# Optimization experiments

Hardware: AMD Instinct MI355X
Metric: run time of the kernel (lower is better)

Reference implementation:

```python
import jax, jax.numpy as jnp
import numpy as np

NEG_SLOPE = 0.2   # PyG GATConv default negative_slope
LN_EPS = 1e-5

B, N, D, HID, HEADS = 4, 10000, 128, 256, 2
F_HEAD = HID // HEADS  # 128
E_RAND = 160000


def setup_inputs() -> dict:
    key = jax.random.key(0)
    ks = jax.random.split(key, 12)
    src = jax.random.randint(ks[0], (E_RAND,), 0, N, dtype=jnp.int32)
    dst = jax.random.randint(ks[1], (E_RAND,), 0, N, dtype=jnp.int32)
    loops = jnp.arange(N, dtype=jnp.int32)  # PyG GATConv adds self-loops
    edge_index = jnp.stack([jnp.concatenate([src, loops]),
                            jnp.concatenate([dst, loops])])  # [2, 170000]
    feature = jax.random.normal(ks[2], (B, N, D), jnp.float32)

    def w(k, shape):
        return jax.random.normal(k, shape, jnp.float32) * 0.05

    return {
        "feature": feature,
        "edge_index": edge_index,
        # layer 1: in D=128 -> heads*F_HEAD = 256
        "W1": w(ks[3], (D, HEADS * F_HEAD)),
        "a_src1": w(ks[4], (HEADS, F_HEAD)),
        "a_dst1": w(ks[5], (HEADS, F_HEAD)),
        "b1": jnp.zeros((HEADS * F_HEAD,), jnp.float32),
        "g1": jnp.ones((HID,), jnp.float32),
        "be1": jnp.zeros((HID,), jnp.float32),
        # layer 2: in 256 -> 256
        "W2": w(ks[6], (HID, HEADS * F_HEAD)),
        "a_src2": w(ks[7], (HEADS, F_HEAD)),
        "a_dst2": w(ks[8], (HEADS, F_HEAD)),
        "b2": jnp.zeros((HEADS * F_HEAD,), jnp.float32),
        "g2": jnp.ones((HID,), jnp.float32),
        "be2": jnp.zeros((HID,), jnp.float32),
    }


def _layer_norm(x, g, b):
    mu = jnp.mean(x, axis=-1, keepdims=True)
    var = jnp.mean(jnp.square(x - mu), axis=-1, keepdims=True)
    return (x - mu) * jax.lax.rsqrt(var + LN_EPS) * g + b


def _gat_conv(x, src, dst, W, a_src, a_dst, b):
    """PyG-style GATConv (concat=True), single graph. x: [N, Din]."""
    n = x.shape[0]
    h = (x @ W).reshape(n, HEADS, F_HEAD)              # [N,H,F]
    al_s = jnp.sum(h * a_src, axis=-1)                  # [N,H]
    al_d = jnp.sum(h * a_dst, axis=-1)                  # [N,H]
    e = jax.nn.leaky_relu(al_s[src] + al_d[dst], NEG_SLOPE)  # [E,H]
    # segment softmax over destination node (self-loops guarantee nonempty)
    m = jax.ops.segment_max(e, dst, num_segments=n)     # [N,H]
    ex = jnp.exp(e - m[dst])
    denom = jax.ops.segment_sum(ex, dst, num_segments=n)
    alpha = ex / (denom[dst] + 1e-16)                   # [E,H]
    msg = h[src] * alpha[..., None]                     # [E,H,F]
    out = jax.ops.segment_sum(msg, dst, num_segments=n) # [N,H,F]
    return out.reshape(n, HEADS * F_HEAD) + b


def reference(feature, edge_index, W1, a_src1, a_dst1, b1, g1, be1,
              W2, a_src2, a_dst2, b2, g2, be2):
    src, dst = edge_index[0], edge_index[1]

    def per_graph(x):
        h = _gat_conv(x, src, dst, W1, a_src1, a_dst1, b1)
        h = jax.nn.relu(_layer_norm(h, g1, be1))  # dropout off (eval)
        h = _gat_conv(h, src, dst, W2, a_src2, a_dst2, b2)
        h = jax.nn.relu(_layer_norm(h, g2, be2))
        return h

    return jax.vmap(per_graph)(feature)  # [B, N, HID]
```

## Files before the change

### kernel.cpp

```cpp
#include <hip/hip_runtime.h>
#include <hip/hip_bf16.h>

#define NN   10000
#define BB   4
#define DD   128
#define HIDD 256
#define NEG  0.2f

using bf16 = __hip_bfloat16;
typedef __bf16 bf16x8 __attribute__((ext_vector_type(8)));
typedef float  f32x4  __attribute__((ext_vector_type(4)));

__device__ __forceinline__ float lrelu(float x) { return x > 0.f ? x : NEG * x; }

__device__ __forceinline__ unsigned pack2(float a, float b) {
    unsigned lo = __bfloat16_as_ushort(__float2bfloat16(a));
    unsigned hi = __bfloat16_as_ushort(__float2bfloat16(b));
    return lo | (hi << 16);
}

__global__ void convert_kernel(const float* __restrict__ x, bf16* __restrict__ y, int n) {
    int i = blockIdx.x * 256 + threadIdx.x;
    if (i < n) y[i] = __float2bfloat16(x[i]);
}

__global__ void convwt_kernel(const float* __restrict__ W, bf16* __restrict__ Wt, int K) {
    int idx = blockIdx.x * 256 + threadIdx.x;
    if (idx < K * HIDD) {
        int k = idx / HIDD, n = idx % HIDD;
        Wt[(size_t)n * K + k] = __float2bfloat16(W[idx]);
    }
}

__global__ void zero_kernel(int* p, int n) {
    int i = blockIdx.x * 256 + threadIdx.x;
    if (i < n) p[i] = 0;
}

__global__ void hist_kernel(const int* __restrict__ dstv, int* counts, int E) {
    int e = blockIdx.x * 256 + threadIdx.x;
    if (e < E) atomicAdd(&counts[dstv[e]], 1);
}

__global__ __launch_bounds__(1024) void scan_kernel(const int* __restrict__ counts,
                                                    int* row_start, int* cursor) {
    __shared__ int part[1024];
    int t = threadIdx.x;
    const int CH = (NN + 1023) / 1024;
    int base = t * CH;
    int s = 0;
    for (int j = 0; j < CH; j++) { int idx = base + j; if (idx < NN) s += counts[idx]; }
    part[t] = s;
    __syncthreads();
    for (int off = 1; off < 1024; off <<= 1) {
        int v = (t >= off) ? part[t - off] : 0;
        __syncthreads();
        part[t] += v;
        __syncthreads();
    }
    int excl = (t == 0) ? 0 : part[t - 1];
    for (int j = 0; j < CH; j++) {
        int idx = base + j;
        if (idx < NN) { row_start[idx] = excl; cursor[idx] = excl; excl += counts[idx]; }
    }
    if (t == 1023) row_start[NN] = part[1023];
}

__global__ void scatter_kernel(const int* __restrict__ srcv, const int* __restrict__ dstv,
                               int* cursor, int* csr_src, int E) {
    int e = blockIdx.x * 256 + threadIdx.x;
    if (e < E) {
        int d = dstv[e];
        int p = atomicAdd(&cursor[d], 1);
        csr_src[p] = srcv[e];
    }
}

template <int K>
__global__ __launch_bounds__(256) void gemm_kernel(const bf16* __restrict__ A,
                                                   const bf16* __restrict__ Wt,
                                                   const float* __restrict__ a_src,
                                                   const float* __restrict__ a_dst,
                                                   bf16* __restrict__ H,
                                                   float* __restrict__ als,
                                                   float* __restrict__ ald) {
    __shared__ bf16 Bs[128 * 128];

    int b    = blockIdx.x;
    int g    = b & 3;
    int r    = b >> 2;
    int head = r & 1;
    int wave = threadIdx.x >> 6;
    int m0   = (r >> 1) * 128 + wave * 32;
    int lane = threadIdx.x & 63;
    int lm   = lane & 15, lq = lane >> 4;

    int rowA = m0 + lm;      if (rowA > NN - 1) rowA = NN - 1;
    int rowB = m0 + 16 + lm; if (rowB > NN - 1) rowB = NN - 1;
    const bf16* Ar0 = A + ((size_t)g * NN + rowA) * K + lq * 8;
    const bf16* Ar1 = A + ((size_t)g * NN + rowB) * K + lq * 8;
    const bf16* Wh  = Wt + (size_t)head * 128 * K;

    f32x4 acc[2][8];
#pragma unroll
    for (int rb = 0; rb < 2; rb++)
#pragma unroll
        for (int i = 0; i < 8; i++) acc[rb][i] = (f32x4){0.f, 0.f, 0.f, 0.f};

    for (int kb = 0; kb < K; kb += 128) {
        if (kb) __syncthreads();
#pragma unroll
        for (int jj = 0; jj < 8; jj++) {
            int j  = wave * 8 + jj;
            int fi = j >> 2, ks = j & 3;
            const bf16* src = Wh + (size_t)(fi * 16 + lm) * K + kb + ks * 32 + lq * 8;
            __builtin_amdgcn_global_load_lds(
                (const __attribute__((address_space(1))) void*)src,
                (__attribute__((address_space(3))) void*)(Bs + j * 512),
                16, 0, 0);
        }
        __syncthreads();

        bf16x8 a0[4], a1[4];
#pragma unroll
        for (int ks = 0; ks < 4; ks++) {
            a0[ks] = *(const bf16x8*)(Ar0 + kb + ks * 32);
            a1[ks] = *(const bf16x8*)(Ar1 + kb + ks * 32);
        }
#pragma unroll
        for (int ks = 0; ks < 4; ks++) {
#pragma unroll
            for (int fi = 0; fi < 8; fi++) {
                bf16x8 bv = *(const bf16x8*)(Bs + ((fi * 4 + ks) * 64 + lane) * 8);
                acc[0][fi] = __builtin_amdgcn_mfma_f32_16x16x32_bf16(a0[ks], bv, acc[0][fi], 0, 0, 0);
                acc[1][fi] = __builtin_amdgcn_mfma_f32_16x16x32_bf16(a1[ks], bv, acc[1][fi], 0, 0, 0);
            }
        }
    }

#pragma unroll
    for (int rb = 0; rb < 2; rb++) {
        int crow0 = m0 + rb * 16 + lq * 4;
        float ps[4] = {0.f, 0.f, 0.f, 0.f};
        float pd[4] = {0.f, 0.f, 0.f, 0.f};
#pragma unroll
        for (int fi = 0; fi < 8; fi++) {
            int col = head * 128 + fi * 16 + lm;
            float as = a_src[col], ad = a_dst[col];
#pragma unroll
            for (int r2 = 0; r2 < 4; r2++) {
                float v = acc[rb][fi][r2];
                ps[r2] = fmaf(v, as, ps[r2]);
                pd[r2] = fmaf(v, ad, pd[r2]);
                int cr = crow0 + r2;
                if (cr < NN)
                    H[((size_t)g * NN + cr) * HIDD + col] = __float2bfloat16(v);
            }
        }
#pragma unroll
        for (int r2 = 0; r2 < 4; r2++) {
            float a = ps[r2], bsum = pd[r2];
#pragma unroll
            for (int off = 1; off < 16; off <<= 1) {
                a += __shfl_xor(a, off);
                bsum += __shfl_xor(bsum, off);
            }
            if (lm == 0) {
                int cr = crow0 + r2;
                if (cr < NN) {
                    als[((size_t)g * NN + cr) * 2 + head] = a;
                    ald[((size_t)g * NN + cr) * 2 + head] = bsum;
                }
            }
        }
    }
}

template <typename OT>
__global__ __launch_bounds__(256) void node_kernel(const int* __restrict__ row_start,
                                                   const int* __restrict__ csr_src,
                                                   const float2* __restrict__ als2,
                                                   const float2* __restrict__ ald2,
                                                   const bf16* __restrict__ H,
                                                   const float* __restrict__ bias,
                                                   const float* __restrict__ gam,
                                                   const float* __restrict__ bet,
                                                   OT* __restrict__ out) {
    int b = blockIdx.x;
    int g = b & 3;
    int wave = threadIdx.x >> 6, lane = threadIdx.x & 63;
    int n = (b >> 2) * 4 + wave;
    if (n >= NN) return;
    int start = row_start[n];
    int deg   = row_start[n + 1] - start;

    int grp = lane >> 5, lch = lane & 31;
    int hd_g = lch >> 4;
    const float* alsf = (const float*)(als2 + (size_t)g * NN);
    float2 ad = ald2[(size_t)g * NN + n];
    float adh = hd_g ? ad.y : ad.x;
    const int* Sr = csr_src + start;
    const bf16* Hg = H + (size_t)g * NN * HIDD;

    float acc[8] = {0.f, 0.f, 0.f, 0.f, 0.f, 0.f, 0.f, 0.f};
    float dsum = 0.f;

#define EDGE_FMA(ss, qq)                                                \
    {                                                                   \
        float wv = __expf(lrelu(alsf[(size_t)(ss) * 2 + hd_g] + adh));  \
        dsum += wv;                                                     \
        acc[0] = fmaf(wv, __uint_as_float(qq.x << 16), acc[0]);         \
        acc[1] = fmaf(wv, __uint_as_float(qq.x & 0xffff0000u), acc[1]); \
        acc[2] = fmaf(wv, __uint_as_float(qq.y << 16), acc[2]);         \
        acc[3] = fmaf(wv, __uint_as_float(qq.y & 0xffff0000u), acc[3]); \
        acc[4] = fmaf(wv, __uint_as_float(qq.z << 16), acc[4]);         \
        acc[5] = fmaf(wv, __uint_as_float(qq.z & 0xffff0000u), acc[5]); \
        acc[6] = fmaf(wv, __uint_as_float(qq.w << 16), acc[6]);         \
        acc[7] = fmaf(wv, __uint_as_float(qq.w & 0xffff0000u), acc[7]); \
    }

    int i = grp;
    for (; i + 6 < deg; i += 8) {
        int s0 = Sr[i], s1 = Sr[i + 2], s2 = Sr[i + 4], s3 = Sr[i + 6];
        uint4 q0 = *(const uint4*)(Hg + (size_t)s0 * HIDD + lch * 8);
        uint4 q1 = *(const uint4*)(Hg + (size_t)s1 * HIDD + lch * 8);
        uint4 q2 = *(const uint4*)(Hg + (size_t)s2 * HIDD + lch * 8);
        uint4 q3 = *(const uint4*)(Hg + (size_t)s3 * HIDD + lch * 8);
        EDGE_FMA(s0, q0)
        EDGE_FMA(s1, q1)
        EDGE_FMA(s2, q2)
        EDGE_FMA(s3, q3)
    }
    for (; i < deg; i += 2) {
        int s0 = Sr[i];
        uint4 q0 = *(const uint4*)(Hg + (size_t)s0 * HIDD + lch * 8);
        EDGE_FMA(s0, q0)
    }
#undef EDGE_FMA

#pragma unroll
    for (int j = 0; j < 8; j++) acc[j] += __shfl_xor(acc[j], 32);
    dsum += __shfl_xor(dsum, 32);
    float rdh = 1.f / dsum;

    float4 bi0 = *(const float4*)(bias + lch * 8);
    float4 bi1 = *(const float4*)(bias + lch * 8 + 4);
    float v[8];
    v[0] = fmaf(acc[0], rdh, bi0.x); v[1] = fmaf(acc[1], rdh, bi0.y);
    v[2] = fmaf(acc[2], rdh, bi0.z); v[3] = fmaf(acc[3], rdh, bi0.w);
    v[4] = fmaf(acc[4], rdh, bi1.x); v[5] = fmaf(acc[5], rdh, bi1.y);
    v[6] = fmaf(acc[6], rdh, bi1.z); v[7] = fmaf(acc[7], rdh, bi1.w);

    float s1 = 0.f, s2 = 0.f;
#pragma unroll
    for (int j = 0; j < 8; j++) { s1 += v[j]; s2 += v[j] * v[j]; }
#pragma unroll
    for (int off = 16; off; off >>= 1) {
        s1 += __shfl_xor(s1, off);
        s2 += __shfl_xor(s2, off);
    }
    float mu  = s1 * (1.f / HIDD);
    float var = s2 * (1.f / HIDD) - mu * mu;
    float rs  = rsqrtf(var + 1e-5f);

    float4 ga0 = *(const float4*)(gam + lch * 8);
    float4 ga1 = *(const float4*)(gam + lch * 8 + 4);
    float4 be0 = *(const float4*)(bet + lch * 8);
    float4 be1 = *(const float4*)(bet + lch * 8 + 4);
    float gaf[8] = {ga0.x, ga0.y, ga0.z, ga0.w, ga1.x, ga1.y, ga1.z, ga1.w};
    float bef[8] = {be0.x, be0.y, be0.z, be0.w, be1.x, be1.y, be1.z, be1.w};

    float o[8];
#pragma unroll
    for (int j = 0; j < 8; j++)
        o[j] = fmaxf((v[j] - mu) * rs * gaf[j] + bef[j], 0.f);

    if (grp == 0) {
        size_t base = ((size_t)g * NN + n) * HIDD + lch * 8;
        if constexpr (sizeof(OT) == 2) {
            uint4 pk;
            pk.x = pack2(o[0], o[1]); pk.y = pack2(o[2], o[3]);
            pk.z = pack2(o[4], o[5]); pk.w = pack2(o[6], o[7]);
            *(uint4*)((bf16*)out + base) = pk;
        } else {
            *(float4*)((float*)out + base)     = make_float4(o[0], o[1], o[2], o[3]);
            *(float4*)((float*)out + base + 4) = make_float4(o[4], o[5], o[6], o[7]);
        }
    }
}

extern "C" void kernel_launch(void* const* d_in, const int* in_sizes, int n_in,
                              void* d_out, int out_size, void* d_ws, size_t ws_size,
                              hipStream_t stream) {
    const float* feature = (const float*)d_in[0];
    const int*   ei      = (const int*)d_in[1];
    const float* W1      = (const float*)d_in[2];
    const float* a_src1  = (const float*)d_in[3];
    const float* a_dst1  = (const float*)d_in[4];
    const float* b1      = (const float*)d_in[5];
    const float* g1      = (const float*)d_in[6];
    const float* be1     = (const float*)d_in[7];
    const float* W2      = (const float*)d_in[8];
    const float* a_src2  = (const float*)d_in[9];
    const float* a_dst2  = (const float*)d_in[10];
    const float* b2      = (const float*)d_in[11];
    const float* g2      = (const float*)d_in[12];
    const float* be2     = (const float*)d_in[13];
    float* out = (float*)d_out;

    const int E = in_sizes[1] / 2;
    const int* srcv = ei;
    const int* dstv = ei + E;

    char* w = (char*)d_ws;
    auto alloc = [&](size_t bytes) -> char* {
        char* p = w;
        w += (bytes + 255) & ~(size_t)255;
        return p;
    };
    int*    counts    = (int*)alloc(sizeof(int) * NN);
    int*    row_start = (int*)alloc(sizeof(int) * (NN + 1));
    int*    cursor    = (int*)alloc(sizeof(int) * NN);
    int*    csr_src   = (int*)alloc(sizeof(int) * E);
    float*  als       = (float*)alloc(sizeof(float) * (size_t)BB * NN * 2);
    float*  ald       = (float*)alloc(sizeof(float) * (size_t)BB * NN * 2);
    bf16*   featbf    = (bf16*)alloc(sizeof(bf16) * (size_t)BB * NN * DD);
    bf16*   h         = (bf16*)alloc(sizeof(bf16) * (size_t)BB * NN * HIDD);
    bf16*   x2        = (bf16*)alloc(sizeof(bf16) * (size_t)BB * NN * HIDD);
    bf16*   Wt        = (bf16*)alloc(sizeof(bf16) * HIDD * HIDD);

    zero_kernel<<<(NN + 255) / 256, 256, 0, stream>>>(counts, NN);
    hist_kernel<<<(E + 255) / 256, 256, 0, stream>>>(dstv, counts, E);
    scan_kernel<<<1, 1024, 0, stream>>>(counts, row_start, cursor);
    scatter_kernel<<<(E + 255) / 256, 256, 0, stream>>>(srcv, dstv, cursor, csr_src, E);

    int nblk = ((NN + 3) / 4) * 4;
    int gblk = 4 * 2 * ((NN + 127) / 128);

    {
        int nf = BB * NN * DD;
        convert_kernel<<<(nf + 255) / 256, 256, 0, stream>>>(feature, featbf, nf);
    }
    convwt_kernel<<<(DD * HIDD + 255) / 256, 256, 0, stream>>>(W1, Wt, DD);
    gemm_kernel<DD><<<gblk, 256, 0, stream>>>(featbf, Wt, a_src1, a_dst1, h, als, ald);
    node_kernel<bf16><<<nblk, 256, 0, stream>>>(row_start, csr_src, (const float2*)als, (const float2*)ald,
                                                h, b1, g1, be1, x2);

    convwt_kernel<<<(HIDD * HIDD + 255) / 256, 256, 0, stream>>>(W2, Wt, HIDD);
    gemm_kernel<HIDD><<<gblk, 256, 0, stream>>>(x2, Wt, a_src2, a_dst2, h, als, ald);
    node_kernel<float><<<nblk, 256, 0, stream>>>(row_start, csr_src, (const float2*)als, (const float2*)ald,
                                                 h, b2, g2, be2, out);
}
```

Baseline: 259.5 us.

## Make GEMM persistent with full weight slice resident in LDS, merge prep kernels

Result: no change. 264.1 us (+1.8%).

```diff
diff --git a/kernel.cpp b/kernel.cpp
--- a/kernel.cpp
+++ b/kernel.cpp
@@ -24,17 +24,22 @@
     if (i < n) y[i] = __float2bfloat16(x[i]);
 }
 
-__global__ void convwt_kernel(const float* __restrict__ W, bf16* __restrict__ Wt, int K) {
+__global__ void prep_kernel(int* counts,
+                            const float* __restrict__ W1, bf16* __restrict__ Wt1,
+                            const float* __restrict__ W2, bf16* __restrict__ Wt2) {
     int idx = blockIdx.x * 256 + threadIdx.x;
-    if (idx < K * HIDD) {
+    if (idx < NN) { counts[idx] = 0; return; }
+    idx -= NN;
+    if (idx < DD * HIDD) {
         int k = idx / HIDD, n = idx % HIDD;
-        Wt[(size_t)n * K + k] = __float2bfloat16(W[idx]);
-    }
-}
-
-__global__ void zero_kernel(int* p, int n) {
-    int i = blockIdx.x * 256 + threadIdx.x;
-    if (i < n) p[i] = 0;
+        Wt1[(size_t)n * DD + k] = __float2bfloat16(W1[idx]);
+        return;
+    }
+    idx -= DD * HIDD;
+    if (idx < HIDD * HIDD) {
+        int k = idx / HIDD, n = idx % HIDD;
+        Wt2[(size_t)n * HIDD + k] = __float2bfloat16(W2[idx]);
+    }
 }
 
 __global__ void hist_kernel(const int* __restrict__ dstv, int* counts, int E) {
@@ -84,93 +89,90 @@
                                                    bf16* __restrict__ H,
                                                    float* __restrict__ als,
                                                    float* __restrict__ ald) {
-    __shared__ bf16 Bs[128 * 128];
-
-    int b    = blockIdx.x;
-    int g    = b & 3;
-    int r    = b >> 2;
-    int head = r & 1;
-    int wave = threadIdx.x >> 6;
-    int m0   = (r >> 1) * 128 + wave * 32;
-    int lane = threadIdx.x & 63;
-    int lm   = lane & 15, lq = lane >> 4;
-
-    int rowA = m0 + lm;      if (rowA > NN - 1) rowA = NN - 1;
-    int rowB = m0 + 16 + lm; if (rowB > NN - 1) rowB = NN - 1;
-    const bf16* Ar0 = A + ((size_t)g * NN + rowA) * K + lq * 8;
-    const bf16* Ar1 = A + ((size_t)g * NN + rowB) * K + lq * 8;
-    const bf16* Wh  = Wt + (size_t)head * 128 * K;
-
-    f32x4 acc[2][8];
-#pragma unroll
-    for (int rb = 0; rb < 2; rb++)
-#pragma unroll
-        for (int i = 0; i < 8; i++) acc[rb][i] = (f32x4){0.f, 0.f, 0.f, 0.f};
-
-    for (int kb = 0; kb < K; kb += 128) {
-        if (kb) __syncthreads();
-#pragma unroll
-        for (int jj = 0; jj < 8; jj++) {
-            int j  = wave * 8 + jj;
-            int fi = j >> 2, ks = j & 3;
-            const bf16* src = Wh + (size_t)(fi * 16 + lm) * K + kb + ks * 32 + lq * 8;
-            __builtin_amdgcn_global_load_lds(
-                (const __attribute__((address_space(1))) void*)src,
-                (__attribute__((address_space(3))) void*)(Bs + j * 512),
-                16, 0, 0);
+    constexpr int NF = K / 32;
+    __shared__ bf16 Bs[8 * NF * 512];
+
+    int b     = blockIdx.x;
+    int g     = b & 3;
+    int r     = b >> 2;
+    int head  = r & 1;
+    int split = r >> 1;
+    int wave  = threadIdx.x >> 6, lane = threadIdx.x & 63;
+    int lm    = lane & 15, lq = lane >> 4;
+
+    const bf16* Wh = Wt + (size_t)head * 128 * K;
+
+#pragma unroll
+    for (int jj = 0; jj < 2 * NF; jj++) {
+        int j  = wave * 2 * NF + jj;
+        int fi = j / NF, ks = j % NF;
+        const bf16* src = Wh + (size_t)(fi * 16 + lm) * K + ks * 32 + lq * 8;
+        __builtin_amdgcn_global_load_lds(
+            (const __attribute__((address_space(1))) void*)src,
+            (__attribute__((address_space(3))) void*)(Bs + j * 512),
+            16, 0, 0);
+    }
+    __syncthreads();
+
+    float4 asv[8], adv[8];
+#pragma unroll
+    for (int fi = 0; fi < 8; fi++) {
+        asv[fi] = *(const float4*)(a_src + head * 128 + fi * 16 + lq * 4);
+        adv[fi] = *(const float4*)(a_dst + head * 128 + fi * 16 + lq * 4);
+    }
+
+    const int NT = (NN + 127) / 128;
+    for (int tt = split; tt < NT; tt += 64) {
+        int m0 = tt * 128 + wave * 32;
+        int rA = min(m0 + lm, NN - 1);
+        int rB = min(m0 + 16 + lm, NN - 1);
+        const bf16* Ar0 = A + ((size_t)g * NN + rA) * K + lq * 8;
+        const bf16* Ar1 = A + ((size_t)g * NN + rB) * K + lq * 8;
+
+        bf16x8 a0[NF], a1[NF];
+#pragma unroll
+        for (int ks = 0; ks < NF; ks++) {
+            a0[ks] = *(const bf16x8*)(Ar0 + ks * 32);
+            a1[ks] = *(const bf16x8*)(Ar1 + ks * 32);
         }
-        __syncthreads();
-
-        bf16x8 a0[4], a1[4];
-#pragma unroll
-        for (int ks = 0; ks < 4; ks++) {
-            a0[ks] = *(const bf16x8*)(Ar0 + kb + ks * 32);
-            a1[ks] = *(const bf16x8*)(Ar1 + kb + ks * 32);
-        }
-#pragma unroll
-        for (int ks = 0; ks < 4; ks++) {
+
+        f32x4 acc[2][8];
+#pragma unroll
+        for (int rb = 0; rb < 2; rb++)
+#pragma unroll
+            for (int i = 0; i < 8; i++) acc[rb][i] = (f32x4){0.f, 0.f, 0.f, 0.f};
+
+#pragma unroll
+        for (int ks = 0; ks < NF; ks++) {
 #pragma unroll
             for (int fi = 0; fi < 8; fi++) {
-                bf16x8 bv = *(const bf16x8*)(Bs + ((fi * 4 + ks) * 64 + lane) * 8);
-                acc[0][fi] = __builtin_amdgcn_mfma_f32_16x16x32_bf16(a0[ks], bv, acc[0][fi], 0, 0, 0);
-                acc[1][fi] = __builtin_amdgcn_mfma_f32_16x16x32_bf16(a1[ks], bv, acc[1][fi], 0, 0, 0);
+                bf16x8 bv = *(const bf16x8*)(Bs + ((size_t)(fi * NF + ks) * 64 + lane) * 8);
+                acc[0][fi] = __builtin_amdgcn_mfma_f32_16x16x32_bf16(bv, a0[ks], acc[0][fi], 0, 0, 0);
+                acc[1][fi] = __builtin_amdgcn_mfma_f32_16x16x32_bf16(bv, a1[ks], acc[1][fi], 0, 0, 0);
             }
         }
-    }
-
-#pragma unroll
-    for (int rb = 0; rb < 2; rb++) {
-        int crow0 = m0 + rb * 16 + lq * 4;
-        float ps[4] = {0.f, 0.f, 0.f, 0.f};
-        float pd[4] = {0.f, 0.f, 0.f, 0.f};
-#pragma unroll
-        for (int fi = 0; fi < 8; fi++) {
-            int col = head * 128 + fi * 16 + lm;
-            float as = a_src[col], ad = a_dst[col];
-#pragma unroll
-            for (int r2 = 0; r2 < 4; r2++) {
-                float v = acc[rb][fi][r2];
-                ps[r2] = fmaf(v, as, ps[r2]);
-                pd[r2] = fmaf(v, ad, pd[r2]);
-                int cr = crow0 + r2;
-                if (cr < NN)
-                    H[((size_t)g * NN + cr) * HIDD + col] = __float2bfloat16(v);
+
+#pragma unroll
+        for (int rb = 0; rb < 2; rb++) {
+            int nd = m0 + rb * 16 + lm;
+            float ps = 0.f, pd = 0.f;
+            bool ok = nd < NN;
+            size_t hb = ((size_t)g * NN + (ok ? nd : 0)) * HIDD + head * 128 + lq * 4;
+#pragma unroll
+            for (int fi = 0; fi < 8; fi++) {
+                f32x4 v = acc[rb][fi];
+                ps += v[0] * asv[fi].x + v[1] * asv[fi].y + v[2] * asv[fi].z + v[3] * asv[fi].w;
+                pd += v[0] * adv[fi].x + v[1] * adv[fi].y + v[2] * adv[fi].z + v[3] * adv[fi].w;
+                if (ok) {
+                    uint2 pk = {pack2(v[0], v[1]), pack2(v[2], v[3])};
+                    *(uint2*)(H + hb + fi * 16) = pk;
+                }
             }
-        }
-#pragma unroll
-        for (int r2 = 0; r2 < 4; r2++) {
-            float a = ps[r2], bsum = pd[r2];
-#pragma unroll
-            for (int off = 1; off < 16; off <<= 1) {
-                a += __shfl_xor(a, off);
-                bsum += __shfl_xor(bsum, off);
-            }
-            if (lm == 0) {
-                int cr = crow0 + r2;
-                if (cr < NN) {
-                    als[((size_t)g * NN + cr) * 2 + head] = a;
-                    ald[((size_t)g * NN + cr) * 2 + head] = bsum;
-                }
+            ps += __shfl_xor(ps, 16); ps += __shfl_xor(ps, 32);
+            pd += __shfl_xor(pd, 16); pd += __shfl_xor(pd, 32);
+            if (lq == 0 && ok) {
+                als[((size_t)g * NN + nd) * 2 + head] = ps;
+                ald[((size_t)g * NN + nd) * 2 + head] = pd;
             }
         }
     }
@@ -327,27 +329,27 @@
     bf16*   featbf    = (bf16*)alloc(sizeof(bf16) * (size_t)BB * NN * DD);
     bf16*   h         = (bf16*)alloc(sizeof(bf16) * (size_t)BB * NN * HIDD);
     bf16*   x2        = (bf16*)alloc(sizeof(bf16) * (size_t)BB * NN * HIDD);
-    bf16*   Wt        = (bf16*)alloc(sizeof(bf16) * HIDD * HIDD);
-
-    zero_kernel<<<(NN + 255) / 256, 256, 0, stream>>>(counts, NN);
+    bf16*   Wt1       = (bf16*)alloc(sizeof(bf16) * DD * HIDD);
+    bf16*   Wt2       = (bf16*)alloc(sizeof(bf16) * HIDD * HIDD);
+
+    int nblk = ((NN + 3) / 4) * 4;
+    int gblk = 4 * 2 * 64;
+
+    {
+        int ptot = NN + DD * HIDD + HIDD * HIDD;
+        prep_kernel<<<(ptot + 255) / 256, 256, 0, stream>>>(counts, W1, Wt1, W2, Wt2);
+        int nf = BB * NN * DD;
+        convert_kernel<<<(nf + 255) / 256, 256, 0, stream>>>(feature, featbf, nf);
+    }
     hist_kernel<<<(E + 255) / 256, 256, 0, stream>>>(dstv, counts, E);
     scan_kernel<<<1, 1024, 0, stream>>>(counts, row_start, cursor);
     scatter_kernel<<<(E + 255) / 256, 256, 0, stream>>>(srcv, dstv, cursor, csr_src, E);
 
-    int nblk = ((NN + 3) / 4) * 4;
-    int gblk = 4 * 2 * ((NN + 127) / 128);
-
-    {
-        int nf = BB * NN * DD;
-        convert_kernel<<<(nf + 255) / 256, 256, 0, stream>>>(feature, featbf, nf);
-    }
-    convwt_kernel<<<(DD * HIDD + 255) / 256, 256, 0, stream>>>(W1, Wt, DD);
-    gemm_kernel<DD><<<gblk, 256, 0, stream>>>(featbf, Wt, a_src1, a_dst1, h, als, ald);
+    gemm_kernel<DD><<<gblk, 256, 0, stream>>>(featbf, Wt1, a_src1, a_dst1, h, als, ald);
     node_kernel<bf16><<<nblk, 256, 0, stream>>>(row_start, csr_src, (const float2*)als, (const float2*)ald,
                                                 h, b1, g1, be1, x2);
 
-    convwt_kernel<<<(HIDD * HIDD + 255) / 256, 256, 0, stream>>>(W2, Wt, HIDD);
-    gemm_kernel<HIDD><<<gblk, 256, 0, stream>>>(x2, Wt, a_src2, a_dst2, h, als, ald);
+    gemm_kernel<HIDD><<<gblk, 256, 0, stream>>>(x2, Wt2, a_src2, a_dst2, h, als, ald);
     node_kernel<float><<<nblk, 256, 0, stream>>>(row_start, csr_src, (const float2*)als, (const float2*)ald,
                                                  h, b2, g2, be2, out);
 }
```
